# Kernel tuning notes

Measured on AMD Instinct MI355X. Metric: run time of the kernel, lower is better.

The kernel has to match this reference:

```python
import jax, jax.numpy as jnp
import numpy as np

D_MODEL = 1024
NUM_HEADS = 16
HEAD_DIM = D_MODEL // NUM_HEADS
THETA = 10000.0
B, S = 1, 2048


def setup_inputs() -> dict:
    key = jax.random.key(0)
    ks = jax.random.split(key, 7)
    sc = 0.02
    return {
        "query": jax.random.normal(ks[0], (B, S, D_MODEL), jnp.float32),
        "key": jax.random.normal(ks[1], (B, S, D_MODEL), jnp.float32),
        "value": jax.random.normal(ks[2], (B, S, D_MODEL), jnp.float32),
        "qkv_w": jax.random.normal(ks[3], (3 * D_MODEL, D_MODEL), jnp.float32) * sc,
        "qkv_b": jax.random.normal(ks[4], (3 * D_MODEL,), jnp.float32) * sc,
        "out_w": jax.random.normal(ks[5], (D_MODEL, D_MODEL), jnp.float32) * sc,
        "out_b": jax.random.normal(ks[6], (D_MODEL,), jnp.float32) * sc,
    }


def _rope_cos_sin(seq_len, head_dim, dtype):
    # freqs_for='lang': inv_freq = theta^(-2i/d), i = 0..d/2-1
    inv_freq = 1.0 / (THETA ** (jnp.arange(0, head_dim, 2, dtype=jnp.float32) / head_dim))
    t = jnp.arange(seq_len, dtype=jnp.float32)
    freqs = jnp.outer(t, inv_freq)                      # [S, d/2]
    emb = jnp.concatenate([freqs, freqs], axis=-1)      # [S, d] (non-interleaved)
    return jnp.cos(emb).astype(dtype), jnp.sin(emb).astype(dtype)


def _rotate_half(x):
    half = x.shape[-1] // 2
    return jnp.concatenate([-x[..., half:], x[..., :half]], axis=-1)


def reference(query, key, value, qkv_w, qkv_b, out_w, out_b):
    # NOTE: module computes q,k,v all from `query` (key/value args unused).
    b, s, d = query.shape
    qkv = query @ qkv_w.T + qkv_b                       # [B,S,3D]
    qkv = qkv.reshape(b, s, 3, NUM_HEADS, HEAD_DIM)
    qkv = jnp.transpose(qkv, (2, 0, 3, 1, 4))           # [3,B,H,S,hd]
    q, k, v = qkv[0], qkv[1], qkv[2]

    cos, sin = _rope_cos_sin(s, HEAD_DIM, query.dtype)  # [S,hd]
    q = q * cos + _rotate_half(q) * sin
    k = k * cos + _rotate_half(k) * sin

    scale = 1.0 / np.sqrt(HEAD_DIM)
    scores = jnp.einsum('bhqd,bhkd->bhqk', q, k) * scale
    attn = jax.nn.softmax(scores, axis=-1)
    ctx = jnp.einsum('bhqk,bhkd->bhqd', attn, v)        # [B,H,S,hd]
    ctx = jnp.transpose(ctx, (0, 2, 1, 3)).reshape(b, s, d)
    return ctx @ out_w.T + out_b
```

## Files before the change

kernel.cpp:

```cpp
#include <hip/hip_runtime.h>
#include <math.h>
#include <stdint.h>

#define SEQ 2048
#define DM  1024
#define NH  16
#define HD  64
#define TRI 3072
#define NSPLIT 2

typedef _Float16 half8 __attribute__((ext_vector_type(8)));
typedef __fp16 fp16x2 __attribute__((ext_vector_type(2)));
typedef float f32x4 __attribute__((ext_vector_type(4)));

#define GLOAD_LDS16(g, l)                                       \
  __builtin_amdgcn_global_load_lds(                             \
      (__attribute__((address_space(1))) void*)(g),             \
      (__attribute__((address_space(3))) void*)(l), 16, 0, 0)

#define QSCALE 0.18033688011112042f

__global__ __launch_bounds__(256)
void cvt3(const float* __restrict__ s1, const float* __restrict__ s2,
          const float* __restrict__ s3, _Float16* __restrict__ d1,
          _Float16* __restrict__ d2, _Float16* __restrict__ d3,
          float2* __restrict__ tab, int n1, int n2) {
  int b = blockIdx.x;
  if (b >= 6144) {
    int i = (b - 6144) * 256 + threadIdx.x;
    int s = i >> 5, d = i & 31;
    float inv = exp2f((float)d * -0.4152410118609203f);
    float ang = (float)s * inv;
    float sn, cs;
    sincosf(ang, &sn, &cs);
    tab[i] = make_float2(cs, sn);
    return;
  }
  int i = (b * 256 + threadIdx.x) * 4;
  const float* s; _Float16* d;
  if (i < n1)            { s = s1; d = d1; }
  else if (i < n1 + n2)  { s = s2; d = d2; i -= n1; }
  else                   { s = s3; d = d3; i -= n1 + n2; }
  float4 v = *(const float4*)(s + i);
  union { _Float16 h[4]; uint2 u; } pk;
  pk.h[0] = (_Float16)v.x; pk.h[1] = (_Float16)v.y;
  pk.h[2] = (_Float16)v.z; pk.h[3] = (_Float16)v.w;
  *(uint2*)(d + i) = pk.u;
}

__global__ __launch_bounds__(256)
void gemm_qkv(const _Float16* __restrict__ A, const _Float16* __restrict__ B,
              const float* __restrict__ bias, const float2* __restrict__ tab,
              _Float16* __restrict__ Qo, _Float16* __restrict__ Ko,
              _Float16* __restrict__ Vo) {
  constexpr int K = DM;
  __shared__ _Float16 As[2][64 * 32];
  __shared__ _Float16 Bs[2][128 * 32];

  const int t = threadIdx.x, lane = t & 63, wv = t >> 6;
  const int l15 = lane & 15, l4 = lane >> 4;
  const int wr = wv >> 1, wc = wv & 1;
  const int bm = blockIdx.y * 64, bn = blockIdx.x * 128;

  auto stage = [&](int buf, int k0) {
    {
      int c = t;
      GLOAD_LDS16(A + (size_t)(bm + (c >> 2)) * K + k0 + (c & 3) * 8,
                  (char*)&As[buf][wv * 512]);
    }
    #pragma unroll
    for (int i = 0; i < 2; ++i) {
      int c = t + i * 256;
      GLOAD_LDS16(B + (size_t)(bn + (c >> 2)) * K + k0 + (c & 3) * 8,
                  (char*)&Bs[buf][(i * 256 + wv * 64) * 8]);
    }
  };

  f32x4 acc[2][4] = {};
  stage(0, 0);
  __syncthreads();

  const int nk = K / 32;
  for (int s = 0; s < nk; ++s) {
    int cur = s & 1;
    if (s + 1 < nk) stage(cur ^ 1, (s + 1) * 32);
    half8 af[2], bf[4];
    #pragma unroll
    for (int mf = 0; mf < 2; ++mf)
      af[mf] = *(const half8*)&As[cur][(wr * 32 + mf * 16 + l15) * 32 + l4 * 8];
    #pragma unroll
    for (int nf = 0; nf < 4; ++nf)
      bf[nf] = *(const half8*)&Bs[cur][(wc * 64 + nf * 16 + l15) * 32 + l4 * 8];
    __builtin_amdgcn_s_setprio(1);
    #pragma unroll
    for (int mf = 0; mf < 2; ++mf)
      #pragma unroll
      for (int nf = 0; nf < 4; ++nf)
        acc[mf][nf] = __builtin_amdgcn_mfma_f32_16x16x32_f16(
            af[mf], bf[nf], acc[mf][nf], 0, 0, 0);
    __builtin_amdgcn_s_setprio(0);
    __syncthreads();
  }

  const int sec = bn >> 10;
  float bv[4];
  #pragma unroll
  for (int nf = 0; nf < 4; ++nf) bv[nf] = bias[bn + wc * 64 + nf * 16 + l15];

  if (sec == 0) {
    #pragma unroll
    for (int mf = 0; mf < 2; ++mf)
      #pragma unroll
      for (int r = 0; r < 4; ++r) {
        int row = bm + wr * 32 + mf * 16 + l4 * 4 + r;
        float v0 = acc[mf][0][r] + bv[0];
        float v1 = acc[mf][1][r] + bv[1];
        float v2 = acc[mf][2][r] + bv[2];
        float v3 = acc[mf][3][r] + bv[3];
        float2 cs0 = tab[row * 32 + l15];
        float2 cs1 = tab[row * 32 + 16 + l15];
        float a0 = (v0 * cs0.x - v2 * cs0.y) * QSCALE;
        float a2 = (v2 * cs0.x + v0 * cs0.y) * QSCALE;
        float a1 = (v1 * cs1.x - v3 * cs1.y) * QSCALE;
        float a3 = (v3 * cs1.x + v1 * cs1.y) * QSCALE;
        _Float16* cr = Qo + (size_t)row * DM + bn + wc * 64 + l15;
        cr[0]  = (_Float16)a0; cr[16] = (_Float16)a1;
        cr[32] = (_Float16)a2; cr[48] = (_Float16)a3;
      }
  } else if (sec == 1) {
    const int hh = ((bn - 1024) >> 6) + wc;
    const int e = l15 & 7, hi = l15 >> 3;
    #pragma unroll
    for (int mf = 0; mf < 2; ++mf)
      #pragma unroll
      for (int r = 0; r < 4; ++r) {
        int row = bm + wr * 32 + mf * 16 + l4 * 4 + r;
        float v0 = acc[mf][0][r] + bv[0];
        float v1 = acc[mf][1][r] + bv[1];
        float v2 = acc[mf][2][r] + bv[2];
        float v3 = acc[mf][3][r] + bv[3];
        float2 cs0 = tab[row * 32 + l15];
        float2 cs1 = tab[row * 32 + 16 + l15];
        float a0 = v0 * cs0.x - v2 * cs0.y;
        float a2 = v2 * cs0.x + v0 * cs0.y;
        float a1 = v1 * cs1.x - v3 * cs1.y;
        float a3 = v3 * cs1.x + v1 * cs1.y;
        int kk = row & 63, kseg = row >> 6, ks7 = kk & 7;
        size_t base = ((size_t)(hh * 32 + kseg) * 64 + kk) * 64;
        Ko[base + (((0 + hi) ^ ks7) * 8) + e] = (_Float16)a0;
        Ko[base + (((2 + hi) ^ ks7) * 8) + e] = (_Float16)a1;
        Ko[base + (((4 + hi) ^ ks7) * 8) + e] = (_Float16)a2;
        Ko[base + (((6 + hi) ^ ks7) * 8) + e] = (_Float16)a3;
      }
  } else {
    const int hh = ((bn - 2048) >> 6) + wc;
    #pragma unroll
    for (int mf = 0; mf < 2; ++mf) {
      int row0 = bm + wr * 32 + mf * 16 + l4 * 4;
      int kk0 = row0 & 63, kseg = row0 >> 6;
      #pragma unroll
      for (int nf = 0; nf < 4; ++nf) {
        int d = nf * 16 + l15;
        union { _Float16 hh4[4]; uint2 u; } pk;
        #pragma unroll
        for (int r = 0; r < 4; ++r)
          pk.hh4[r] = (_Float16)(acc[mf][nf][r] + bv[nf]);
        size_t off = ((size_t)(hh * 32 + kseg) * 64 + d) * 64 +
                     (((kk0 >> 3) ^ (d & 7)) * 8) + (kk0 & 7);
        *(uint2*)(Vo + off) = pk.u;
      }
    }
  }
}

__global__ __launch_bounds__(256)
void gemm_out(const _Float16* __restrict__ A, const _Float16* __restrict__ B,
              const float* __restrict__ bias, float* __restrict__ C) {
  constexpr int K = DM, N = DM;
  __shared__ _Float16 As[2][64 * 32];
  __shared__ _Float16 Bs[2][128 * 32];

  const int t = threadIdx.x, lane = t & 63, wv = t >> 6;
  const int l15 = lane & 15, l4 = lane >> 4;
  const int wr = wv >> 1, wc = wv & 1;
  const int bm = blockIdx.y * 64, bn = blockIdx.x * 128;

  auto stage = [&](int buf, int k0) {
    {
      int c = t;
      GLOAD_LDS16(A + (size_t)(bm + (c >> 2)) * K + k0 + (c & 3) * 8,
                  (char*)&As[buf][wv * 512]);
    }
    #pragma unroll
    for (int i = 0; i < 2; ++i) {
      int c = t + i * 256;
      GLOAD_LDS16(B + (size_t)(bn + (c >> 2)) * K + k0 + (c & 3) * 8,
                  (char*)&Bs[buf][(i * 256 + wv * 64) * 8]);
    }
  };

  f32x4 acc[2][4] = {};
  stage(0, 0);
  __syncthreads();

  const int nk = K / 32;
  for (int s = 0; s < nk; ++s) {
    int cur = s & 1;
    if (s + 1 < nk) stage(cur ^ 1, (s + 1) * 32);
    half8 af[2], bf[4];
    #pragma unroll
    for (int mf = 0; mf < 2; ++mf)
      af[mf] = *(const half8*)&As[cur][(wr * 32 + mf * 16 + l15) * 32 + l4 * 8];
    #pragma unroll
    for (int nf = 0; nf < 4; ++nf)
      bf[nf] = *(const half8*)&Bs[cur][(wc * 64 + nf * 16 + l15) * 32 + l4 * 8];
    __builtin_amdgcn_s_setprio(1);
    #pragma unroll
    for (int mf = 0; mf < 2; ++mf)
      #pragma unroll
      for (int nf = 0; nf < 4; ++nf)
        acc[mf][nf] = __builtin_amdgcn_mfma_f32_16x16x32_f16(
            af[mf], bf[nf], acc[mf][nf], 0, 0, 0);
    __builtin_amdgcn_s_setprio(0);
    __syncthreads();
  }

  float bv[4];
  #pragma unroll
  for (int nf = 0; nf < 4; ++nf) bv[nf] = bias[bn + wc * 64 + nf * 16 + l15];
  #pragma unroll
  for (int mf = 0; mf < 2; ++mf)
    #pragma unroll
    for (int r = 0; r < 4; ++r) {
      int row = bm + wr * 32 + mf * 16 + l4 * 4 + r;
      float* cr = C + (size_t)row * N + bn + wc * 64 + l15;
      cr[0]  = acc[mf][0][r] + bv[0];
      cr[16] = acc[mf][1][r] + bv[1];
      cr[32] = acc[mf][2][r] + bv[2];
      cr[48] = acc[mf][3][r] + bv[3];
    }
}

__global__ __launch_bounds__(256)
void attn_f16(const _Float16* __restrict__ Qg, const _Float16* __restrict__ Kg,
              const _Float16* __restrict__ Vg, _Float16* __restrict__ po,
              float* __restrict__ pl) {
  __shared__ _Float16 Kl[2][64 * 64];
  __shared__ _Float16 Vt[2][64 * 64];
  __shared__ _Float16 Pl[4][1024];

  const int t = threadIdx.x, lane = t & 63, wv = t >> 6;
  const int l15 = lane & 15, l4 = lane >> 4;
  const int bid = blockIdx.x;
  const int c = bid & 31, qb = bid >> 5;
  const int h = c & 15, z = c >> 4;
  const int q0 = qb * 64;
  const int seg0 = z * (SEQ / NSPLIT / 64);

  const _Float16* Qp = Qg + h * HD;
  const _Float16* Kbase = Kg + (size_t)h * 32 * 4096;
  const _Float16* Vbase = Vg + (size_t)h * 32 * 4096;

  half8 qf[2];
  {
    const _Float16* qrow = Qp + (size_t)(q0 + wv * 16 + l15) * DM;
    qf[0] = *(const half8*)(qrow + l4 * 8);
    qf[1] = *(const half8*)(qrow + 32 + l4 * 8);
  }

  auto issueKV = [&](int buf, int seg) {
    const _Float16* ks = Kbase + (size_t)seg * 4096;
    const _Float16* vs = Vbase + (size_t)seg * 4096;
    GLOAD_LDS16(ks + (size_t)t * 8,         (char*)&Kl[buf][(wv * 64) * 8]);
    GLOAD_LDS16(ks + (size_t)(t + 256) * 8, (char*)&Kl[buf][(256 + wv * 64) * 8]);
    GLOAD_LDS16(vs + (size_t)t * 8,         (char*)&Vt[buf][(wv * 64) * 8]);
    GLOAD_LDS16(vs + (size_t)(t + 256) * 8, (char*)&Vt[buf][(256 + wv * 64) * 8]);
  };

  f32x4 lacc = {0.f, 0.f, 0.f, 0.f};
  f32x4 o[4] = {};
  char* Pw = (char*)Pl[wv];

  issueKV(0, seg0);

  const int NT = SEQ / NSPLIT / 64;
  for (int tt = 0; tt < NT; ++tt) {
    const int cur = tt & 1;
    const bool pf = (tt + 1 < NT);
    if (pf) {
      issueKV(cur ^ 1, seg0 + tt + 1);
      asm volatile("s_waitcnt vmcnt(4)" ::: "memory");
    } else {
      asm volatile("s_waitcnt vmcnt(0)" ::: "memory");
    }
    __builtin_amdgcn_s_barrier();
    __builtin_amdgcn_sched_barrier(0);

    f32x4 sT[4] = {};
    __builtin_amdgcn_s_setprio(1);
    #pragma unroll
    for (int ds = 0; ds < 2; ++ds)
      #pragma unroll
      for (int mf = 0; mf < 4; ++mf) {
        int r = mf * 16 + l15;
        int cb = ds * 4 + l4;
        half8 kf = *(const half8*)(&Kl[cur][r * 64 + ((cb ^ (r & 7)) * 8)]);
        sT[mf] = __builtin_amdgcn_mfma_f32_16x16x32_f16(kf, qf[ds], sT[mf], 0, 0, 0);
      }
    __builtin_amdgcn_s_setprio(0);

    #pragma unroll
    for (int mf = 0; mf < 4; ++mf) {
      f32x4 p;
      #pragma unroll
      for (int r = 0; r < 4; ++r) p[r] = exp2f(sT[mf][r] - 8.0f);
      lacc += p;
      union { fp16x2 h[2]; uint2 u; } pu;
      pu.h[0] = __builtin_amdgcn_cvt_pkrtz(p[0], p[1]);
      pu.h[1] = __builtin_amdgcn_cvt_pkrtz(p[2], p[3]);
      int cc = (mf * 2 + (l4 >> 1)) ^ (l15 & 7);
      *(uint2*)(Pw + l15 * 128 + cc * 16 + (l4 & 1) * 8) = pu.u;
    }

    __builtin_amdgcn_s_setprio(1);
    #pragma unroll
    for (int ks = 0; ks < 2; ++ks) {
      half8 pa = *(const half8*)(Pw + l15 * 128 +
                                 (((ks * 4 + l4) ^ (l15 & 7)) * 16));
      #pragma unroll
      for (int nf = 0; nf < 4; ++nf) {
        int d = nf * 16 + l15;
        half8 vb = *(const half8*)((char*)Vt[cur] + d * 128 +
                                   (((ks * 4 + l4) ^ (d & 7)) * 16));
        o[nf] = __builtin_amdgcn_mfma_f32_16x16x32_f16(pa, vb, o[nf], 0, 0, 0);
      }
    }
    __builtin_amdgcn_s_setprio(0);

    __builtin_amdgcn_s_barrier();
  }

  float lv = (lacc[0] + lacc[1]) + (lacc[2] + lacc[3]);
  lv += __shfl_xor(lv, 16);
  lv += __shfl_xor(lv, 32);
  _Float16* pz = po + (size_t)z * SEQ * DM;
  #pragma unroll
  for (int nf = 0; nf < 4; ++nf)
    #pragma unroll
    for (int r = 0; r < 4; ++r) {
      int row = q0 + wv * 16 + l4 * 4 + r;
      int col = h * HD + nf * 16 + l15;
      pz[(size_t)row * DM + col] = (_Float16)o[nf][r];
    }
  if (l4 == 0) {
    int q = q0 + wv * 16 + l15;
    pl[(z * NH + h) * SEQ + q] = lv;
  }
}

__global__ __launch_bounds__(256)
void merge2(const _Float16* __restrict__ po, const float* __restrict__ pl,
            _Float16* __restrict__ ctx) {
  int e = (blockIdx.x * 256 + threadIdx.x) * 8;
  int s = e >> 10, h = (e & 1023) >> 6;
  int idx = h * SEQ + s;
  float inv = 1.0f / (pl[idx] + pl[NH * SEQ + idx]);
  half8 a = *(const half8*)(po + e);
  half8 b = *(const half8*)(po + (size_t)SEQ * DM + e);
  half8 o;
  #pragma unroll
  for (int j = 0; j < 8; ++j)
    o[j] = (_Float16)(((float)a[j] + (float)b[j]) * inv);
  *(half8*)(ctx + e) = o;
}

extern "C" void kernel_launch(void* const* d_in, const int* in_sizes, int n_in,
                              void* d_out, int out_size, void* d_ws, size_t ws_size,
                              hipStream_t stream) {
  const float* query = (const float*)d_in[0];
  const float* qkv_w = (const float*)d_in[3];
  const float* qkv_b = (const float*)d_in[4];
  const float* out_w = (const float*)d_in[5];
  const float* out_b = (const float*)d_in[6];
  float* out = (float*)d_out;

  _Float16* Aq   = (_Float16*)d_ws;
  _Float16* Wqkv = Aq + (size_t)SEQ * DM;
  _Float16* Wout = Wqkv + (size_t)TRI * DM;
  _Float16* Qb   = Wout + (size_t)DM * DM;
  _Float16* Kb   = Qb + (size_t)SEQ * DM;
  _Float16* Vb   = Kb + (size_t)SEQ * DM;
  _Float16* ctx  = Vb + (size_t)SEQ * DM;
  float2*   tab  = (float2*)(ctx + (size_t)SEQ * DM);
  _Float16* po = (_Float16*)d_ws;
  float*    pl = (float*)((char*)d_ws + (8u << 20));

  cvt3<<<6400, 256, 0, stream>>>(query, qkv_w, out_w, Aq, Wqkv, Wout, tab,
                                 SEQ * DM, TRI * DM);

  gemm_qkv<<<dim3(TRI / 128, SEQ / 64), 256, 0, stream>>>(
      Aq, Wqkv, qkv_b, tab, Qb, Kb, Vb);

  attn_f16<<<(SEQ / 64) * NH * NSPLIT, 256, 0, stream>>>(Qb, Kb, Vb, po, pl);

  merge2<<<SEQ * DM / 8 / 256, 256, 0, stream>>>(po, pl, ctx);

  gemm_out<<<dim3(DM / 128, SEQ / 64), 256, 0, stream>>>(ctx, Wout, out_b, out);
}
```

Before: 98.90 us.

## Keep softmax probabilities in registers and feed PV MFMA directly, drop LDS staging

The attention kernel now keeps the fp16 probability fragments in registers and uses them directly as the A operand of 16x16x16 MFMAs, with V read in a matching swizzled layout. This removes the per-wave LDS P buffer, its write/read round trip, and the trailing barrier. The K/V prefetch is now issued after the barrier with a full vmcnt(0) wait, which gives a single barrier per tile but less overlap of loads. The -8 exponent offset is also dropped, which changes fp16 overflow headroom.

```diff
diff --git a/kernel.cpp b/kernel.cpp
--- a/kernel.cpp
+++ b/kernel.cpp
@@ -10,6 +10,7 @@
 #define NSPLIT 2
 
 typedef _Float16 half8 __attribute__((ext_vector_type(8)));
+typedef _Float16 half4 __attribute__((ext_vector_type(4)));
 typedef __fp16 fp16x2 __attribute__((ext_vector_type(2)));
 typedef float f32x4 __attribute__((ext_vector_type(4)));
 
@@ -247,7 +248,6 @@
               float* __restrict__ pl) {
   __shared__ _Float16 Kl[2][64 * 64];
   __shared__ _Float16 Vt[2][64 * 64];
-  __shared__ _Float16 Pl[4][1024];
 
   const int t = threadIdx.x, lane = t & 63, wv = t >> 6;
   const int l15 = lane & 15, l4 = lane >> 4;
@@ -279,22 +279,17 @@
 
   f32x4 lacc = {0.f, 0.f, 0.f, 0.f};
   f32x4 o[4] = {};
-  char* Pw = (char*)Pl[wv];
 
   issueKV(0, seg0);
 
   const int NT = SEQ / NSPLIT / 64;
+  #pragma unroll 2
   for (int tt = 0; tt < NT; ++tt) {
     const int cur = tt & 1;
-    const bool pf = (tt + 1 < NT);
-    if (pf) {
-      issueKV(cur ^ 1, seg0 + tt + 1);
-      asm volatile("s_waitcnt vmcnt(4)" ::: "memory");
-    } else {
-      asm volatile("s_waitcnt vmcnt(0)" ::: "memory");
-    }
+    asm volatile("s_waitcnt vmcnt(0)" ::: "memory");
     __builtin_amdgcn_s_barrier();
     __builtin_amdgcn_sched_barrier(0);
+    if (tt + 1 < NT) issueKV(cur ^ 1, seg0 + tt + 1);
 
     f32x4 sT[4] = {};
     __builtin_amdgcn_s_setprio(1);
@@ -309,35 +304,30 @@
       }
     __builtin_amdgcn_s_setprio(0);
 
+    half4 pA[4];
     #pragma unroll
     for (int mf = 0; mf < 4; ++mf) {
       f32x4 p;
       #pragma unroll
-      for (int r = 0; r < 4; ++r) p[r] = exp2f(sT[mf][r] - 8.0f);
+      for (int r = 0; r < 4; ++r) p[r] = exp2f(sT[mf][r]);
       lacc += p;
-      union { fp16x2 h[2]; uint2 u; } pu;
-      pu.h[0] = __builtin_amdgcn_cvt_pkrtz(p[0], p[1]);
-      pu.h[1] = __builtin_amdgcn_cvt_pkrtz(p[2], p[3]);
-      int cc = (mf * 2 + (l4 >> 1)) ^ (l15 & 7);
-      *(uint2*)(Pw + l15 * 128 + cc * 16 + (l4 & 1) * 8) = pu.u;
+      union { fp16x2 h2[2]; half4 a; } pu;
+      pu.h2[0] = __builtin_amdgcn_cvt_pkrtz(p[0], p[1]);
+      pu.h2[1] = __builtin_amdgcn_cvt_pkrtz(p[2], p[3]);
+      pA[mf] = pu.a;
     }
 
     __builtin_amdgcn_s_setprio(1);
     #pragma unroll
-    for (int ks = 0; ks < 2; ++ks) {
-      half8 pa = *(const half8*)(Pw + l15 * 128 +
-                                 (((ks * 4 + l4) ^ (l15 & 7)) * 16));
+    for (int mf = 0; mf < 4; ++mf) {
+      int cc = ((mf * 2 + (l4 >> 1)) ^ (l15 & 7)) * 16 + (l4 & 1) * 8;
       #pragma unroll
       for (int nf = 0; nf < 4; ++nf) {
-        int d = nf * 16 + l15;
-        half8 vb = *(const half8*)((char*)Vt[cur] + d * 128 +
-                                   (((ks * 4 + l4) ^ (d & 7)) * 16));
-        o[nf] = __builtin_amdgcn_mfma_f32_16x16x32_f16(pa, vb, o[nf], 0, 0, 0);
+        half4 vb = *(const half4*)((char*)Vt[cur] + (nf * 16 + l15) * 128 + cc);
+        o[nf] = __builtin_amdgcn_mfma_f32_16x16x16f16(pA[mf], vb, o[nf], 0, 0, 0);
       }
     }
     __builtin_amdgcn_s_setprio(0);
-
-    __builtin_amdgcn_s_barrier();
   }
 
   float lv = (lacc[0] + lacc[1]) + (lacc[2] + lacc[3]);
```

Result: no change. 97.73 us (-1.2%).
